# Kernel optimization log

Measured on AMD Instinct MI355X. Metric: run time of the kernel, lower is better.

Reference implementation:

```python
import jax, jax.numpy as jnp
import numpy as np

N, E, G = 50000, 400000, 512
F_IN, H = 128, 128  # OPS_LENGTH, hidden_channels
NEG_SLOPE = 0.2
BN_EPS = 1e-5


def seg_softmax(e, idx, n):
    m = jax.ops.segment_max(e, idx, num_segments=n)
    ex = jnp.exp(e - m[idx])
    s = jax.ops.segment_sum(ex, idx, num_segments=n)
    return ex / (s[idx] + 1e-16)


def gatv2(x, src, dst, Wl, Wr, att, b, n):
    # PyG GATv2Conv, heads=1: e = att . leaky_relu(Wl x_src + Wr x_dst),
    # alpha = softmax over incoming edges per dst, out = sum alpha * Wl x_src + b
    xl = x @ Wl
    xr = x @ Wr
    z = jax.nn.leaky_relu(xl[src] + xr[dst], NEG_SLOPE)  # [E, out]
    e = jnp.einsum('ed,d->e', z, att)
    a = seg_softmax(e, dst, n)
    return jax.ops.segment_sum(xl[src] * a[:, None], dst, num_segments=n) + b


def bn_eval(x, g, b, m, v):
    return (x - m) * jax.lax.rsqrt(v + BN_EPS) * g + b


def setup_inputs() -> dict:
    key = jax.random.key(0)
    ks = jax.random.split(key, 40)
    d = {}
    d['x'] = jax.random.normal(ks[0], (N, F_IN), dtype=jnp.float32)
    d['edge_index'] = jax.random.randint(ks[1], (2, E), 0, N)
    d['batch'] = jnp.sort(jax.random.randint(ks[2], (N,), 0, G))
    def lin(k, i, o, s=None):
        s = s if s is not None else 1.0 / np.sqrt(i)
        return jax.random.normal(k, (i, o), dtype=jnp.float32) * s
    # conv1: 128->128, conv2: 128->256, conv3: 256->128
    d['Wl1'] = lin(ks[3], F_IN, H); d['Wr1'] = lin(ks[4], F_IN, H)
    d['att1'] = jax.random.normal(ks[5], (H,), dtype=jnp.float32) * 0.1
    d['b1'] = jnp.zeros((H,), jnp.float32)
    d['Wl2'] = lin(ks[6], H, 2 * H); d['Wr2'] = lin(ks[7], H, 2 * H)
    d['att2'] = jax.random.normal(ks[8], (2 * H,), dtype=jnp.float32) * 0.1
    d['b2'] = jnp.zeros((2 * H,), jnp.float32)
    d['Wl3'] = lin(ks[9], 2 * H, H); d['Wr3'] = lin(ks[10], 2 * H, H)
    d['att3'] = jax.random.normal(ks[11], (H,), dtype=jnp.float32) * 0.1
    d['b3'] = jnp.zeros((H,), jnp.float32)
    d['Wlin1'] = lin(ks[12], H, 128); d['blin1'] = jnp.zeros((128,), jnp.float32)
    d['Wlin2'] = lin(ks[13], 128, 64); d['blin2'] = jnp.zeros((64,), jnp.float32)
    d['Wlin3'] = lin(ks[14], 64, 2); d['blin3'] = jnp.zeros((2,), jnp.float32)
    for name, dim, i in [('bng', H, 15), ('bn1', 128, 19), ('bn2', 64, 23)]:
        d[name + '_g'] = jax.random.uniform(ks[i], (dim,), minval=0.5, maxval=1.5)
        d[name + '_b'] = jax.random.normal(ks[i + 1], (dim,), dtype=jnp.float32) * 0.1
        d[name + '_m'] = jax.random.normal(ks[i + 2], (dim,), dtype=jnp.float32) * 0.1
        d[name + '_v'] = jax.random.uniform(ks[i + 3], (dim,), minval=0.5, maxval=1.5)
    return d


def reference(x, edge_index, batch, Wl1, Wr1, att1, b1, Wl2, Wr2, att2, b2,
              Wl3, Wr3, att3, b3, Wlin1, blin1, Wlin2, blin2, Wlin3, blin3,
              bng_g, bng_b, bng_m, bng_v, bn1_g, bn1_b, bn1_m, bn1_v,
              bn2_g, bn2_b, bn2_m, bn2_v):
    src, dst = edge_index[0], edge_index[1]
    h = jax.nn.relu(gatv2(x, src, dst, Wl1, Wr1, att1, b1, N))
    h = jax.nn.relu(gatv2(h, src, dst, Wl2, Wr2, att2, b2, N))
    h = gatv2(h, src, dst, Wl3, Wr3, att3, b3, N)
    # global_mean_pool
    sums = jax.ops.segment_sum(h, batch, num_segments=G)
    cnt = jax.ops.segment_sum(jnp.ones((N,), h.dtype), batch, num_segments=G)
    g = sums / jnp.maximum(cnt, 1.0)[:, None]
    # dropout p=0.5 is identity in eval mode; BatchNorms in eval mode
    g = bn_eval(g, bng_g, bng_b, bng_m, bng_v)
    g = bn_eval(jax.nn.relu(g @ Wlin1 + blin1), bn1_g, bn1_b, bn1_m, bn1_v)
    g = bn_eval(jax.nn.relu(g @ Wlin2 + blin2), bn2_g, bn2_b, bn2_m, bn2_v)
    return jax.nn.relu(g @ Wlin3 + blin3)
```

## Files before the change

### kernel.cpp

```cpp
#include <hip/hip_runtime.h>
#include <math.h>

#define N_NODES 50000
#define N_EDGES 400000
#define N_GRAPHS 512
#define NEG_SLOPE 0.2f
#define BN_EPS 1e-5f
#define SCAN_BLOCKS 49

#define C6 0.8656170245333781f
#define C4 0.5770780163555854f
#define THR_LOG2 11.541560327111708f

typedef __attribute__((ext_vector_type(8))) short bf16x8;
typedef __attribute__((ext_vector_type(4))) float f32x4;

__device__ __forceinline__ ushort f2b(float f) {
    unsigned u = __float_as_uint(f);
    unsigned r = (u + 0x7fffu + ((u >> 16) & 1u)) >> 16;
    return (ushort)r;
}
__device__ __forceinline__ float b2f(ushort u) {
    return __uint_as_float((unsigned)u << 16);
}

__global__ void cvt_kernel(const float* __restrict__ in, ushort* __restrict__ out,
                           int total4) {
    const int i = blockIdx.x * 256 + threadIdx.x;
    if (i >= total4) return;
    float4 v = *(const float4*)(in + (size_t)i * 4);
    ushort4 o;
    o.x = f2b(v.x); o.y = f2b(v.y); o.z = f2b(v.z); o.w = f2b(v.w);
    *(ushort4*)(out + (size_t)i * 4) = o;
}

__global__ void wcvt_all_kernel(const float* __restrict__ Wl1, const float* __restrict__ Wr1,
                                const float* __restrict__ Wl2, const float* __restrict__ Wr2,
                                const float* __restrict__ Wl3, const float* __restrict__ Wr3,
                                ushort* __restrict__ wt1, ushort* __restrict__ wt2,
                                ushort* __restrict__ wt3) {
    const int i = blockIdx.x * 256 + threadIdx.x;
    if (i < 32768) {
        const int m = i >> 7, k = i & 127;
        const float v = (m < 128) ? Wl1[k * 128 + m] : Wr1[k * 128 + (m - 128)];
        wt1[i] = f2b(v);
    } else if (i < 98304) {
        const int j = i - 32768;
        const int m = j >> 7, k = j & 127;
        const float v = (m < 256) ? Wl2[k * 256 + m] : Wr2[k * 256 + (m - 256)];
        wt2[j] = f2b(v);
    } else if (i < 163840) {
        const int j = i - 98304;
        const int m = j >> 8, k = j & 255;
        const float v = (m < 128) ? Wl3[k * 128 + m] : Wr3[k * 128 + (m - 128)];
        wt3[j] = f2b(v);
    }
}

__global__ __launch_bounds__(256) void gemm_bf16_kernel(
    const ushort* __restrict__ A, const ushort* __restrict__ Bt,
    ushort* __restrict__ C, int n, int K, int M) {
    __shared__ ushort As[128][40];
    __shared__ ushort Bs[128][40];
    const int tid = threadIdx.x;
    const int row0 = blockIdx.x * 128;
    const int col0 = blockIdx.y * 128;
    const int w = tid >> 6, lane = tid & 63;
    const int wr = (w >> 1) * 64, wc = (w & 1) * 64;
    const int lr = lane & 15, kg = lane >> 4;

    const int srow = tid >> 1, shalf = tid & 1;

    f32x4 acc[4][4];
#pragma unroll
    for (int i = 0; i < 4; ++i)
#pragma unroll
        for (int j = 0; j < 4; ++j) acc[i][j] = (f32x4){0.f, 0.f, 0.f, 0.f};

    for (int k0 = 0; k0 < K; k0 += 32) {
        {
            const int gr = row0 + srow;
            uint4 v0 = make_uint4(0, 0, 0, 0), v1 = v0;
            if (gr < n) {
                const uint4* p = (const uint4*)(A + (size_t)gr * K + k0) + shalf * 2;
                v0 = p[0]; v1 = p[1];
            }
            uint4* d = (uint4*)&As[srow][shalf * 16];
            d[0] = v0; d[1] = v1;
            const int gb = col0 + srow;
            const uint4* p = (const uint4*)(Bt + (size_t)gb * K + k0) + shalf * 2;
            uint4* db = (uint4*)&Bs[srow][shalf * 16];
            db[0] = p[0]; db[1] = p[1];
        }
        __syncthreads();
        bf16x8 af[4], bfr[4];
#pragma unroll
        for (int mi = 0; mi < 4; ++mi)
            af[mi] = *(const bf16x8*)&As[wr + mi * 16 + lr][kg * 8];
#pragma unroll
        for (int ni = 0; ni < 4; ++ni)
            bfr[ni] = *(const bf16x8*)&Bs[wc + ni * 16 + lr][kg * 8];
#pragma unroll
        for (int mi = 0; mi < 4; ++mi)
#pragma unroll
            for (int ni = 0; ni < 4; ++ni)
                acc[mi][ni] = __builtin_amdgcn_mfma_f32_16x16x32_bf16(
                    af[mi], bfr[ni], acc[mi][ni], 0, 0, 0);
        __syncthreads();
    }
#pragma unroll
    for (int mi = 0; mi < 4; ++mi)
#pragma unroll
        for (int ni = 0; ni < 4; ++ni)
#pragma unroll
            for (int j = 0; j < 4; ++j) {
                const int r = row0 + wr + mi * 16 + kg * 4 + j;
                if (r < n)
                    C[(size_t)r * M + col0 + wc + ni * 16 + lr] = f2b(acc[mi][ni][j]);
            }
}

__global__ void deg_count_kernel(const int* __restrict__ ei, int* __restrict__ deg) {
    const int e = blockIdx.x * 256 + threadIdx.x;
    if (e < N_EDGES) atomicAdd(&deg[ei[N_EDGES + e]], 1);
}

__global__ __launch_bounds__(256) void scanA_kernel(const int* __restrict__ deg,
                                                    int* __restrict__ rowp,
                                                    int* __restrict__ bsum) {
    const int t = threadIdx.x, b = blockIdx.x;
    const int i0 = b * 1024 + t * 4;
    int4 d = make_int4(0, 0, 0, 0);
    if (i0 + 3 < N_NODES) d = *(const int4*)(deg + i0);
    else {
        if (i0 + 0 < N_NODES) d.x = deg[i0 + 0];
        if (i0 + 1 < N_NODES) d.y = deg[i0 + 1];
        if (i0 + 2 < N_NODES) d.z = deg[i0 + 2];
    }
    const int tsum = d.x + d.y + d.z + d.w;
    int inc = tsum;
    const int lane = t & 63, wave = t >> 6;
#pragma unroll
    for (int o = 1; o < 64; o <<= 1) {
        int v = __shfl_up(inc, o, 64);
        if (lane >= o) inc += v;
    }
    __shared__ int wsum[4];
    if (lane == 63) wsum[wave] = inc;
    __syncthreads();
    int wbase = 0;
#pragma unroll
    for (int ww = 0; ww < 4; ++ww)
        if (ww < wave) wbase += wsum[ww];
    const int texcl = wbase + inc - tsum;
    int4 o4;
    o4.x = texcl;
    o4.y = o4.x + d.x;
    o4.z = o4.y + d.y;
    o4.w = o4.z + d.z;
    if (i0 + 3 < N_NODES) *(int4*)(rowp + i0) = o4;
    else {
        if (i0 + 0 < N_NODES) rowp[i0 + 0] = o4.x;
        if (i0 + 1 < N_NODES) rowp[i0 + 1] = o4.y;
        if (i0 + 2 < N_NODES) rowp[i0 + 2] = o4.z;
    }
    if (t == 255) bsum[b] = wbase + inc;
}

__global__ __launch_bounds__(256) void scanC_kernel(const int* __restrict__ bsum,
                                                    int* __restrict__ rowp) {
    const int t = threadIdx.x, b = blockIdx.x;
    __shared__ int base_s;
    if (t < 64) {
        int v = (t < b) ? bsum[t] : 0;
#pragma unroll
        for (int o = 32; o; o >>= 1) v += __shfl_xor(v, o, 64);
        if (t == 0) base_s = v;
    }
    __syncthreads();
    const int base = base_s;
    const int i0 = b * 1024 + t * 4;
    if (base != 0) {
        if (i0 + 3 < N_NODES) {
            int4 v = *(int4*)(rowp + i0);
            v.x += base; v.y += base; v.z += base; v.w += base;
            *(int4*)(rowp + i0) = v;
        } else {
            if (i0 + 0 < N_NODES) rowp[i0 + 0] += base;
            if (i0 + 1 < N_NODES) rowp[i0 + 1] += base;
            if (i0 + 2 < N_NODES) rowp[i0 + 2] += base;
        }
    }
    if (b == 0 && t == 0) rowp[N_NODES] = N_EDGES;
}

__global__ void csr_fill_kernel(const int* __restrict__ ei, const int* __restrict__ rowp,
                                int* __restrict__ cursor, int* __restrict__ csr_src) {
    const int e = blockIdx.x * 256 + threadIdx.x;
    if (e >= N_EDGES) return;
    const int d = ei[N_EDGES + e];
    const int pos = atomicAdd(&cursor[d], 1);
    csr_src[rowp[d] + pos] = ei[e];
}

template <int VEC>
__device__ __forceinline__ void sm_upd(float& m, float& s, float* acc, float p,
                                       const float* l) {
    if (p > m + THR_LOG2) {
        const float sc = __builtin_amdgcn_exp2f(m - p);
        s = s * sc + 1.f;
#pragma unroll
        for (int k = 0; k < VEC; ++k) acc[k] = acc[k] * sc + l[k];
        m = p;
    } else {
        const float w = __builtin_amdgcn_exp2f(p - m);
        s += w;
#pragma unroll
        for (int k = 0; k < VEC; ++k) acc[k] += w * l[k];
    }
}

template <int FO, int VEC>
__device__ __forceinline__ float edge_dot(const ushort* __restrict__ hx, int src, int co,
                                          const float* a6, const float* a4,
                                          const float* r, float* l) {
    if constexpr (VEC == 4) {
        ushort4 t = *(const ushort4*)(hx + (size_t)src * (2 * FO) + co);
        l[0] = b2f(t.x); l[1] = b2f(t.y); l[2] = b2f(t.z); l[3] = b2f(t.w);
    } else {
        ushort2 t = *(const ushort2*)(hx + (size_t)src * (2 * FO) + co);
        l[0] = b2f(t.x); l[1] = b2f(t.y);
    }
    float p = 0.f;
#pragma unroll
    for (int k = 0; k < VEC; ++k) {
        const float z = l[k] + r[k];
        p = fmaf(a6[k], z, p);
        p = fmaf(a4[k], fabsf(z), p);
    }
    return p;
}

template <int FO, int VEC>
__global__ __launch_bounds__(256) void gat_edge_kernel(
    const int* __restrict__ rowp, const int* __restrict__ csr_src,
    const ushort* __restrict__ hx,
    const float* __restrict__ att, const float* __restrict__ bias,
    float* __restrict__ outf, ushort* __restrict__ outb, int do_relu) {
    const int d = blockIdx.x * 4 + (threadIdx.x >> 6);
    const int lane = threadIdx.x & 63;
    if (d >= N_NODES) return;
    const int co = lane * VEC;

    float a6[VEC], a4[VEC], r[VEC];
    if constexpr (VEC == 4) {
        float4 t4 = *(const float4*)(att + co);
        a6[0] = C6 * t4.x; a6[1] = C6 * t4.y; a6[2] = C6 * t4.z; a6[3] = C6 * t4.w;
        a4[0] = C4 * t4.x; a4[1] = C4 * t4.y; a4[2] = C4 * t4.z; a4[3] = C4 * t4.w;
        ushort4 u4 = *(const ushort4*)(hx + (size_t)d * (2 * FO) + FO + co);
        r[0] = b2f(u4.x); r[1] = b2f(u4.y); r[2] = b2f(u4.z); r[3] = b2f(u4.w);
    } else {
        float2 t2 = *(const float2*)(att + co);
        a6[0] = C6 * t2.x; a6[1] = C6 * t2.y;
        a4[0] = C4 * t2.x; a4[1] = C4 * t2.y;
        ushort2 u2 = *(const ushort2*)(hx + (size_t)d * (2 * FO) + FO + co);
        r[0] = b2f(u2.x); r[1] = b2f(u2.y);
    }

    const int jb = rowp[d], je = rowp[d + 1];
    float m0 = -INFINITY, s0 = 0.f, m1 = -INFINITY, s1 = 0.f;
    float acc0[VEC] = {}, acc1[VEC] = {};

    int j = jb;
    for (; j + 3 < je; j += 4) {
        const int sA = csr_src[j + 0];
        const int sB = csr_src[j + 1];
        const int sC = csr_src[j + 2];
        const int sD = csr_src[j + 3];
        float lA[VEC], lB[VEC], lC[VEC], lD[VEC];
        float pA = edge_dot<FO, VEC>(hx, sA, co, a6, a4, r, lA);
        float pB = edge_dot<FO, VEC>(hx, sB, co, a6, a4, r, lB);
        float pC = edge_dot<FO, VEC>(hx, sC, co, a6, a4, r, lC);
        float pD = edge_dot<FO, VEC>(hx, sD, co, a6, a4, r, lD);
#pragma unroll
        for (int o = 32; o; o >>= 1) {
            pA += __shfl_xor(pA, o, 64);
            pB += __shfl_xor(pB, o, 64);
            pC += __shfl_xor(pC, o, 64);
            pD += __shfl_xor(pD, o, 64);
        }
        sm_upd<VEC>(m0, s0, acc0, pA, lA);
        sm_upd<VEC>(m1, s1, acc1, pB, lB);
        sm_upd<VEC>(m0, s0, acc0, pC, lC);
        sm_upd<VEC>(m1, s1, acc1, pD, lD);
    }
    for (; j < je; ++j) {
        const int sA = csr_src[j];
        float lA[VEC];
        float pA = edge_dot<FO, VEC>(hx, sA, co, a6, a4, r, lA);
#pragma unroll
        for (int o = 32; o; o >>= 1) pA += __shfl_xor(pA, o, 64);
        sm_upd<VEC>(m0, s0, acc0, pA, lA);
    }

    float s, acc[VEC];
    if (je > jb) {
        const float M = fmaxf(m0, m1);
        const float sc0 = __builtin_amdgcn_exp2f(m0 - M);
        const float sc1 = __builtin_amdgcn_exp2f(m1 - M);
        s = s0 * sc0 + s1 * sc1;
#pragma unroll
        for (int k = 0; k < VEC; ++k) acc[k] = acc0[k] * sc0 + acc1[k] * sc1;
    } else {
        s = 0.f;
#pragma unroll
        for (int k = 0; k < VEC; ++k) acc[k] = 0.f;
    }

    const float inv = 1.f / (s + 1e-16f);
#pragma unroll
    for (int k = 0; k < VEC; ++k) {
        float v = acc[k] * inv + bias[co + k];
        if (do_relu) v = fmaxf(v, 0.f);
        acc[k] = v;
    }
    if (outf) {
        if constexpr (VEC == 4)
            *(float4*)(outf + (size_t)d * FO + co) = make_float4(acc[0], acc[1], acc[2], acc[3]);
        else
            *(float2*)(outf + (size_t)d * FO + co) = make_float2(acc[0], acc[1]);
    }
    if (outb) {
        if constexpr (VEC == 4) {
            ushort4 o; o.x = f2b(acc[0]); o.y = f2b(acc[1]); o.z = f2b(acc[2]); o.w = f2b(acc[3]);
            *(ushort4*)(outb + (size_t)d * FO + co) = o;
        } else {
            ushort2 o; o.x = f2b(acc[0]); o.y = f2b(acc[1]);
            *(ushort2*)(outb + (size_t)d * FO + co) = o;
        }
    }
}

__global__ void gstart_kernel(const int* __restrict__ batch, int* __restrict__ gstart) {
    const int i = blockIdx.x * 256 + threadIdx.x;
    if (i >= N_NODES) return;
    const int b = batch[i];
    if (i == 0) {
        for (int g = 0; g <= b; ++g) gstart[g] = 0;
    } else {
        const int pb = batch[i - 1];
        for (int g = pb + 1; g <= b; ++g) gstart[g] = i;
    }
    if (i == N_NODES - 1) {
        for (int g = b + 1; g <= N_GRAPHS; ++g) gstart[g] = N_NODES;
    }
}

__global__ __launch_bounds__(128) void pool2_kernel(const float* __restrict__ h,
                                                    const int* __restrict__ gstart,
                                                    float* __restrict__ gsum,
                                                    float* __restrict__ gcnt) {
    const int g = blockIdx.x, t = threadIdx.x;
    const int b = gstart[g], e = gstart[g + 1];
    float s = 0.f;
    for (int i = b; i < e; ++i) s += h[(size_t)i * 128 + t];
    gsum[g * 128 + t] = s;
    if (t == 0) gcnt[g] = (float)(e - b);
}

__global__ __launch_bounds__(128) void mlp_kernel(
    const float* __restrict__ gsum, const float* __restrict__ gcnt,
    const float* __restrict__ W1, const float* __restrict__ b1,
    const float* __restrict__ W2, const float* __restrict__ b2,
    const float* __restrict__ W3, const float* __restrict__ b3,
    const float* __restrict__ bng_g, const float* __restrict__ bng_b,
    const float* __restrict__ bng_m, const float* __restrict__ bng_v,
    const float* __restrict__ bn1_g, const float* __restrict__ bn1_b,
    const float* __restrict__ bn1_m, const float* __restrict__ bn1_v,
    const float* __restrict__ bn2_g, const float* __restrict__ bn2_b,
    const float* __restrict__ bn2_m, const float* __restrict__ bn2_v,
    float* __restrict__ out) {
    __shared__ float s0[128], s1[128], s2[64];
    const int g = blockIdx.x, t = threadIdx.x;
    const float cnt = fmaxf(gcnt[g], 1.f);
    float v = gsum[g * 128 + t] / cnt;
    v = (v - bng_m[t]) * rsqrtf(bng_v[t] + BN_EPS) * bng_g[t] + bng_b[t];
    s0[t] = v;
    __syncthreads();
    float a1 = b1[t];
    for (int i = 0; i < 128; ++i) a1 += s0[i] * W1[i * 128 + t];
    a1 = fmaxf(a1, 0.f);
    a1 = (a1 - bn1_m[t]) * rsqrtf(bn1_v[t] + BN_EPS) * bn1_g[t] + bn1_b[t];
    s1[t] = a1;
    __syncthreads();
    if (t < 64) {
        float a2 = b2[t];
        for (int i = 0; i < 128; ++i) a2 += s1[i] * W2[i * 64 + t];
        a2 = fmaxf(a2, 0.f);
        a2 = (a2 - bn2_m[t]) * rsqrtf(bn2_v[t] + BN_EPS) * bn2_g[t] + bn2_b[t];
        s2[t] = a2;
    }
    __syncthreads();
    if (t < 2) {
        float a3 = b3[t];
        for (int i = 0; i < 64; ++i) a3 += s2[i] * W3[i * 2 + t];
        out[g * 2 + t] = fmaxf(a3, 0.f);
    }
}

extern "C" void kernel_launch(void* const* d_in, const int* in_sizes, int n_in,
                              void* d_out, int out_size, void* d_ws, size_t ws_size,
                              hipStream_t stream) {
    const float* x = (const float*)d_in[0];
    const int* ei = (const int*)d_in[1];
    const int* batch = (const int*)d_in[2];
    const float* Wl1 = (const float*)d_in[3];
    const float* Wr1 = (const float*)d_in[4];
    const float* att1 = (const float*)d_in[5];
    const float* b1 = (const float*)d_in[6];
    const float* Wl2 = (const float*)d_in[7];
    const float* Wr2 = (const float*)d_in[8];
    const float* att2 = (const float*)d_in[9];
    const float* b2 = (const float*)d_in[10];
    const float* Wl3 = (const float*)d_in[11];
    const float* Wr3 = (const float*)d_in[12];
    const float* att3 = (const float*)d_in[13];
    const float* b3 = (const float*)d_in[14];
    const float* Wlin1 = (const float*)d_in[15];
    const float* blin1 = (const float*)d_in[16];
    const float* Wlin2 = (const float*)d_in[17];
    const float* blin2 = (const float*)d_in[18];
    const float* Wlin3 = (const float*)d_in[19];
    const float* blin3 = (const float*)d_in[20];
    const float* bng_g = (const float*)d_in[21];
    const float* bng_b = (const float*)d_in[22];
    const float* bng_m = (const float*)d_in[23];
    const float* bng_v = (const float*)d_in[24];
    const float* bn1_g = (const float*)d_in[25];
    const float* bn1_b = (const float*)d_in[26];
    const float* bn1_m = (const float*)d_in[27];
    const float* bn1_v = (const float*)d_in[28];
    const float* bn2_g = (const float*)d_in[29];
    const float* bn2_b = (const float*)d_in[30];
    const float* bn2_m = (const float*)d_in[31];
    const float* bn2_v = (const float*)d_in[32];

    float* ws = (float*)d_ws;
    ushort* hx = (ushort*)ws;
    float* h3 = (float*)(hx + (size_t)N_NODES * 512);
    ushort* hbf = (ushort*)(h3 + (size_t)N_NODES * 128);
    ushort* wt1 = hbf + (size_t)N_NODES * 256;
    ushort* wt2 = wt1 + 256 * 128;
    ushort* wt3 = wt2 + 512 * 128;
    int* deg = (int*)(wt3 + 256 * 256);
    int* cursor = deg + N_NODES;
    int* rowp = cursor + N_NODES;
    int* csr_src = rowp + N_NODES + 1;
    int* gstart = csr_src + N_EDGES;
    int* bsum = gstart + N_GRAPHS + 1;
    float* gsum = (float*)(bsum + SCAN_BLOCKS);
    float* gcnt = gsum + (size_t)N_GRAPHS * 128;

    const int eb = (N_EDGES + 255) / 256;

    hipMemsetAsync(deg, 0, (size_t)N_NODES * 2 * 4, stream);
    deg_count_kernel<<<eb, 256, 0, stream>>>(ei, deg);
    scanA_kernel<<<SCAN_BLOCKS, 256, 0, stream>>>(deg, rowp, bsum);
    scanC_kernel<<<SCAN_BLOCKS, 256, 0, stream>>>(bsum, rowp);
    csr_fill_kernel<<<eb, 256, 0, stream>>>(ei, rowp, cursor, csr_src);
    gstart_kernel<<<(N_NODES + 255) / 256, 256, 0, stream>>>(batch, gstart);

    wcvt_all_kernel<<<640, 256, 0, stream>>>(Wl1, Wr1, Wl2, Wr2, Wl3, Wr3, wt1, wt2, wt3);
    cvt_kernel<<<(N_NODES * 128 / 4 + 255) / 256, 256, 0, stream>>>(
        x, hbf, N_NODES * 128 / 4);

    const int nb = (N_NODES + 3) / 4;
    const int gx = (N_NODES + 127) / 128;

    gemm_bf16_kernel<<<dim3(gx, 2), 256, 0, stream>>>(hbf, wt1, hx, N_NODES, 128, 256);
    gat_edge_kernel<128, 2><<<nb, 256, 0, stream>>>(rowp, csr_src, hx,
                                                    att1, b1, nullptr, hbf, 1);
    gemm_bf16_kernel<<<dim3(gx, 4), 256, 0, stream>>>(hbf, wt2, hx, N_NODES, 128, 512);
    gat_edge_kernel<256, 4><<<nb, 256, 0, stream>>>(rowp, csr_src, hx,
                                                    att2, b2, nullptr, hbf, 1);
    gemm_bf16_kernel<<<dim3(gx, 2), 256, 0, stream>>>(hbf, wt3, hx, N_NODES, 256, 256);
    gat_edge_kernel<128, 2><<<nb, 256, 0, stream>>>(rowp, csr_src, hx,
                                                    att3, b3, h3, nullptr, 0);

    pool2_kernel<<<N_GRAPHS, 128, 0, stream>>>(h3, gstart, gsum, gcnt);

    mlp_kernel<<<N_GRAPHS, 128, 0, stream>>>(
        gsum, gcnt, Wlin1, blin1, Wlin2, blin2, Wlin3, blin3,
        bng_g, bng_b, bng_m, bng_v, bn1_g, bn1_b, bn1_m, bn1_v,
        bn2_g, bn2_b, bn2_m, bn2_v, (float*)d_out);
}
```

Measured before the change: 304.9 us.

## Load GEMM tiles directly into LDS with XOR swizzle and padded rows

New measurement: 297.0 us. 1.03x faster.

```diff
diff --git a/kernel.cpp b/kernel.cpp
--- a/kernel.cpp
+++ b/kernel.cpp
@@ -2,6 +2,7 @@
 #include <math.h>
 
 #define N_NODES 50000
+#define NPAD 50048
 #define N_EDGES 400000
 #define N_GRAPHS 512
 #define NEG_SLOPE 0.2f
@@ -22,6 +23,12 @@
 }
 __device__ __forceinline__ float b2f(ushort u) {
     return __uint_as_float((unsigned)u << 16);
+}
+
+__device__ __forceinline__ void gld_lds16(const void* g, void* l) {
+    __builtin_amdgcn_global_load_lds(
+        (const __attribute__((address_space(1))) void*)g,
+        (__attribute__((address_space(3))) void*)l, 16, 0, 0);
 }
 
 __global__ void cvt_kernel(const float* __restrict__ in, ushort* __restrict__ out,
@@ -59,9 +66,9 @@
 
 __global__ __launch_bounds__(256) void gemm_bf16_kernel(
     const ushort* __restrict__ A, const ushort* __restrict__ Bt,
-    ushort* __restrict__ C, int n, int K, int M) {
-    __shared__ ushort As[128][40];
-    __shared__ ushort Bs[128][40];
+    ushort* __restrict__ C, int K, int M) {
+    __shared__ ushort As[4096];
+    __shared__ ushort Bs[4096];
     const int tid = threadIdx.x;
     const int row0 = blockIdx.x * 128;
     const int col0 = blockIdx.y * 128;
@@ -69,7 +76,29 @@
     const int wr = (w >> 1) * 64, wc = (w & 1) * 64;
     const int lr = lane & 15, kg = lane >> 4;
 
-    const int srow = tid >> 1, shalf = tid & 1;
+    char* as_b = (char*)As;
+    char* bs_b = (char*)Bs;
+
+    const int o0 = tid * 16;
+    const int o1 = o0 + 4096;
+    const int u0 = o0 ^ ((o0 >> 3) & 0x30);
+    const int u1 = o1 ^ ((o1 >> 3) & 0x30);
+    const int ar0 = u0 >> 6, ac0 = (u0 >> 4) & 3;
+    const int ar1 = (u1 >> 6) & 127, ac1 = (u1 >> 4) & 3;
+
+    const ushort* ga0 = A + (size_t)(row0 + ar0) * K + ac0 * 8;
+    const ushort* ga1 = A + (size_t)(row0 + ar1) * K + ac1 * 8;
+    const ushort* gb0 = Bt + (size_t)(col0 + ar0) * K + ac0 * 8;
+    const ushort* gb1 = Bt + (size_t)(col0 + ar1) * K + ac1 * 8;
+
+    char* da0 = as_b + w * 1024;
+    char* da1 = as_b + 4096 + w * 1024;
+    char* db0 = bs_b + w * 1024;
+    char* db1 = bs_b + 4096 + w * 1024;
+
+    const int sxor = ((lr >> 1) & 3) << 4;
+    const int abase = (((wr + lr) * 64) + kg * 16) ^ sxor;
+    const int bbase = (((wc + lr) * 64) + kg * 16) ^ sxor;
 
     f32x4 acc[4][4];
 #pragma unroll
@@ -78,28 +107,19 @@
         for (int j = 0; j < 4; ++j) acc[i][j] = (f32x4){0.f, 0.f, 0.f, 0.f};
 
     for (int k0 = 0; k0 < K; k0 += 32) {
-        {
-            const int gr = row0 + srow;
-            uint4 v0 = make_uint4(0, 0, 0, 0), v1 = v0;
-            if (gr < n) {
-                const uint4* p = (const uint4*)(A + (size_t)gr * K + k0) + shalf * 2;
-                v0 = p[0]; v1 = p[1];
-            }
-            uint4* d = (uint4*)&As[srow][shalf * 16];
-            d[0] = v0; d[1] = v1;
-            const int gb = col0 + srow;
-            const uint4* p = (const uint4*)(Bt + (size_t)gb * K + k0) + shalf * 2;
-            uint4* db = (uint4*)&Bs[srow][shalf * 16];
-            db[0] = p[0]; db[1] = p[1];
-        }
+        gld_lds16(ga0, da0);
+        gld_lds16(ga1, da1);
+        gld_lds16(gb0, db0);
+        gld_lds16(gb1, db1);
+        ga0 += 32; ga1 += 32; gb0 += 32; gb1 += 32;
         __syncthreads();
         bf16x8 af[4], bfr[4];
 #pragma unroll
         for (int mi = 0; mi < 4; ++mi)
-            af[mi] = *(const bf16x8*)&As[wr + mi * 16 + lr][kg * 8];
+            af[mi] = *(const bf16x8*)(as_b + abase + mi * 1024);
 #pragma unroll
         for (int ni = 0; ni < 4; ++ni)
-            bfr[ni] = *(const bf16x8*)&Bs[wc + ni * 16 + lr][kg * 8];
+            bfr[ni] = *(const bf16x8*)(bs_b + bbase + ni * 1024);
 #pragma unroll
         for (int mi = 0; mi < 4; ++mi)
 #pragma unroll
@@ -115,8 +135,7 @@
 #pragma unroll
             for (int j = 0; j < 4; ++j) {
                 const int r = row0 + wr + mi * 16 + kg * 4 + j;
-                if (r < n)
-                    C[(size_t)r * M + col0 + wc + ni * 16 + lr] = f2b(acc[mi][ni][j]);
+                C[(size_t)r * M + col0 + wc + ni * 16 + lr] = f2b(acc[mi][ni][j]);
             }
 }
 
@@ -447,9 +466,9 @@
 
     float* ws = (float*)d_ws;
     ushort* hx = (ushort*)ws;
-    float* h3 = (float*)(hx + (size_t)N_NODES * 512);
+    float* h3 = (float*)(hx + (size_t)NPAD * 512);
     ushort* hbf = (ushort*)(h3 + (size_t)N_NODES * 128);
-    ushort* wt1 = hbf + (size_t)N_NODES * 256;
+    ushort* wt1 = hbf + (size_t)NPAD * 256;
     ushort* wt2 = wt1 + 256 * 128;
     ushort* wt3 = wt2 + 512 * 128;
     int* deg = (int*)(wt3 + 256 * 256);
@@ -475,15 +494,15 @@
         x, hbf, N_NODES * 128 / 4);
 
     const int nb = (N_NODES + 3) / 4;
-    const int gx = (N_NODES + 127) / 128;
-
-    gemm_bf16_kernel<<<dim3(gx, 2), 256, 0, stream>>>(hbf, wt1, hx, N_NODES, 128, 256);
+    const int gx = NPAD / 128;
+
+    gemm_bf16_kernel<<<dim3(gx, 2), 256, 0, stream>>>(hbf, wt1, hx, 128, 256);
     gat_edge_kernel<128, 2><<<nb, 256, 0, stream>>>(rowp, csr_src, hx,
                                                     att1, b1, nullptr, hbf, 1);
-    gemm_bf16_kernel<<<dim3(gx, 4), 256, 0, stream>>>(hbf, wt2, hx, N_NODES, 128, 512);
+    gemm_bf16_kernel<<<dim3(gx, 4), 256, 0, stream>>>(hbf, wt2, hx, 128, 512);
     gat_edge_kernel<256, 4><<<nb, 256, 0, stream>>>(rowp, csr_src, hx,
                                                     att2, b2, nullptr, hbf, 1);
-    gemm_bf16_kernel<<<dim3(gx, 2), 256, 0, stream>>>(hbf, wt3, hx, N_NODES, 256, 256);
+    gemm_bf16_kernel<<<dim3(gx, 2), 256, 0, stream>>>(hbf, wt3, hx, 256, 256);
     gat_edge_kernel<128, 2><<<nb, 256, 0, stream>>>(rowp, csr_src, hx,
                                                     att3, b3, h3, nullptr, 0);
 
```
